# Kernel optimization log

Hardware: AMD Instinct MI355X
Metric: run time of the kernel (lower is better)

## Reference

```python
import jax, jax.numpy as jnp
import numpy as np

N_WAY, K_SHOT = 5, 1
N_CLASSES = 64
D = 8


def _conv(x, w, b):
    y = jax.lax.conv_general_dilated(x, w, (2, 2), 'SAME',
                                     dimension_numbers=('NCHW', 'OIHW', 'NCHW'))
    return jax.nn.relu(y + b[None, :, None, None])


def setup_inputs() -> dict:
    key = jax.random.key(0)
    ks = jax.random.split(key, 12)
    b, s_sup, q, h, w = 4, N_WAY * K_SHOT, 1, 64, 64
    rnd = lambda k, shape: jax.random.normal(k, shape, jnp.float32) * 0.05
    return {
        'support_x': jax.random.normal(ks[0], (b, s_sup, 3, h, w), jnp.float32),
        'support_y': jax.random.randint(ks[1], (b, s_sup), 0, N_CLASSES),
        'query_x': jax.random.normal(ks[2], (b, q, 3, h, w), jnp.float32),
        'query_y': jax.random.randint(ks[3], (b, q), 0, N_CLASSES),
        'k1': rnd(ks[4], (32, 3, 3, 3)), 'bc1': jnp.zeros((32,), jnp.float32),
        'k2': rnd(ks[5], (48, 32, 3, 3)), 'bc2': jnp.zeros((48,), jnp.float32),
        'k3': rnd(ks[6], (64, 48, 3, 3)), 'bc3': jnp.zeros((64,), jnp.float32),
        'Wlog': rnd(ks[7], (64, N_CLASSES)), 'blog': jnp.zeros((N_CLASSES,), jnp.float32),
        'Wg1': rnd(ks[8], (132, 128)), 'bg1': jnp.zeros((128,), jnp.float32),
        'Wg2': rnd(ks[9], (128, 64)), 'bg2': jnp.zeros((64,), jnp.float32),
        'Wf1': rnd(ks[10], (64, 16)), 'bf1': jnp.zeros((16,), jnp.float32),
        'Wf2': rnd(ks[11], (16, 1)), 'bf2': jnp.zeros((1,), jnp.float32),
    }


def reference(support_x, support_y, query_x, query_y,
              k1, bc1, k2, bc2, k3, bc3, Wlog, blog,
              Wg1, bg1, Wg2, bg2, Wf1, bf1, Wf2, bf2):
    x = jnp.concatenate([support_x, query_x], axis=1)       # [b, s, 3, h, w]
    label = jnp.concatenate([support_y, query_y], axis=1)   # [b, s]
    b, s = label.shape
    h, w = x.shape[-2:]

    feat = x.reshape(b * s, 3, h, w)
    feat = _conv(feat, k1, bc1)
    feat = _conv(feat, k2, bc2)
    feat = _conv(feat, k3, bc3)                              # [b*s, c, D, D]
    c = feat.shape[1]
    logits = feat.mean(axis=(2, 3)) @ Wlog + blog            # [b*s, n_classes]

    # --- append normalized (i/d, j/d) coord channels ---
    ii = jnp.arange(D, dtype=feat.dtype) / D
    coord = jnp.stack([jnp.broadcast_to(ii[:, None], (D, D)),
                       jnp.broadcast_to(ii[None, :], (D, D))])        # [2, D, D]
    feat = feat.reshape(b, s, c, D, D)
    feat = jnp.concatenate([feat, jnp.broadcast_to(coord, (b, s, 2, D, D))], axis=2)
    c2 = c + 2
    m = D * D
    a = feat.reshape(b, s, c2, m).transpose(0, 1, 3, 2)      # [b, s, m, c2]

    # --- relation network g over all (set-pair, position-pair) combos ---
    # original: g(concat(x_i, x_j)) where x_i = x[b, j, :, q], x_j = x[b, i, :, p]
    # split first linear: concat @ Wg1 = x_i @ Wg1[:c2] + x_j @ Wg1[c2:]
    W1a, W1b = Wg1[:c2], Wg1[c2:]
    u = a @ W1a                                              # [b, s_j, m_q, 128]
    v = a @ W1b + bg1                                        # [b, s_i, m_p, 128]
    # hdd[b,i,j,q,p] = relu(u[b,j,q] + v[b,i,p])  -> [b, s, s, m, m, 128]
    hdd = jax.nn.relu(u[:, None, :, :, None, :] + v[:, :, None, None, :, :])
    g = jax.nn.relu(hdd @ Wg2 + bg2)                         # [b, s, s, m, m, 64]
    x_f = g.sum(axis=(3, 4))                                 # [b, s, s, 64]
    score = jax.nn.sigmoid(jax.nn.relu(x_f @ Wf1 + bf1) @ Wf2 + bf2)  # [b, s, s, 1]

    # --- losses ---
    logp = jax.nn.log_softmax(logits, axis=-1)
    lab = label.reshape(-1)
    cls_loss = -jnp.take_along_axis(logp, lab[:, None], axis=1).mean()

    y = (label[:, :, None] == label[:, None, :])[..., None].astype(score.dtype)
    P = score[..., 0]                                        # [b, s, s]
    Pt = P.transpose(0, 2, 1)
    sym, anti = 0.5 * (P + Pt), 0.5 * (P - Pt)
    sym_n = jnp.sqrt((sym ** 2).sum(axis=(1, 2)))            # Frobenius per batch
    anti_n = jnp.sqrt((anti ** 2).sum(axis=(1, 2)))
    sym_loss = ((sym_n - anti_n) / (sym_n + anti_n)).mean()
    euc_loss = ((score - y) ** 2).mean()
    rn_loss = euc_loss - 0.1 * sym_loss
    return (cls_loss, rn_loss, sym_loss)
```

## Files before the change

kernel.cpp:

```cpp
#include <hip/hip_runtime.h>

typedef _Float16 f16x8 __attribute__((ext_vector_type(8)));
typedef float f32x4 __attribute__((ext_vector_type(4)));

__global__ void conv1_k(const float* __restrict__ sx, const float* __restrict__ qx,
                        const float* __restrict__ w, const float* __restrict__ bias,
                        float* __restrict__ out,
                        const float* __restrict__ Wg2, _Float16* __restrict__ W2h) {
    if (blockIdx.x == 768) {
        for (int s = 0; s < 4; s++) {
            int slot = threadIdx.x + 256*s;
            int tile = slot >> 6, lane = slot & 63;
            int kt = tile >> 2, nt = tile & 3;
            int quad = lane >> 4, col = lane & 15;
            f16x8 t;
            #pragma unroll
            for (int jj = 0; jj < 8; jj++)
                t[jj] = (_Float16)Wg2[(kt*32 + quad*8 + jj)*64 + nt*16 + col];
            *(f16x8*)&W2h[slot*8] = t;
        }
        return;
    }
    int n  = blockIdx.x >> 5;
    int oc = blockIdx.x & 31;
    int bi = n / 6, si = n % 6;
    const float* inp = (si < 5) ? sx + (size_t)((bi*5+si)*3)*4096
                                : qx + (size_t)(bi*3)*4096;
    __shared__ float wl[27];
    __shared__ float bl;
    if (threadIdx.x < 27) wl[threadIdx.x] = w[oc*27 + threadIdx.x];
    if (threadIdx.x == 0) bl = bias[oc];
    __syncthreads();
    for (int idx = threadIdx.x; idx < 1024; idx += 256) {
        int oy = idx >> 5, ox = idx & 31;
        float acc = bl;
        #pragma unroll
        for (int ic = 0; ic < 3; ic++) {
            const float* ip = inp + ic*4096;
            #pragma unroll
            for (int dy = 0; dy < 3; dy++) {
                int iy = 2*oy + dy;
                if (iy >= 64) continue;
                #pragma unroll
                for (int dx = 0; dx < 3; dx++) {
                    int ix = 2*ox + dx;
                    if (ix >= 64) continue;
                    acc += ip[iy*64+ix] * wl[ic*9 + dy*3 + dx];
                }
            }
        }
        out[(size_t)(n*32+oc)*1024 + idx] = fmaxf(acc, 0.f);
    }
}

__global__ void conv2_k(const float* __restrict__ in, const float* __restrict__ w,
                        const float* __restrict__ bias, float* __restrict__ out) {
    int n   = blockIdx.x / 12;
    int ocg = blockIdx.x % 12;
    __shared__ float wl[4*32*9];
    for (int e = threadIdx.x; e < 1152; e += 256) wl[e] = w[ocg*4*288 + e];
    __syncthreads();
    int oy = threadIdx.x >> 4, ox = threadIdx.x & 15;
    float a0 = bias[ocg*4+0], a1 = bias[ocg*4+1], a2 = bias[ocg*4+2], a3 = bias[ocg*4+3];
    const float* ib = in + (size_t)n*32*1024;
    for (int ic = 0; ic < 32; ic++) {
        const float* ip = ib + ic*1024;
        float tap[9];
        #pragma unroll
        for (int dy = 0; dy < 3; dy++)
            #pragma unroll
            for (int dx = 0; dx < 3; dx++) {
                int iy = 2*oy+dy, ix = 2*ox+dx;
                tap[dy*3+dx] = (iy < 32 && ix < 32) ? ip[iy*32+ix] : 0.f;
            }
        #pragma unroll
        for (int t = 0; t < 9; t++) {
            a0 += tap[t]*wl[0*288 + ic*9 + t];
            a1 += tap[t]*wl[1*288 + ic*9 + t];
            a2 += tap[t]*wl[2*288 + ic*9 + t];
            a3 += tap[t]*wl[3*288 + ic*9 + t];
        }
    }
    size_t ob = (size_t)(n*48 + ocg*4)*256 + threadIdx.x;
    out[ob        ] = fmaxf(a0, 0.f);
    out[ob + 256  ] = fmaxf(a1, 0.f);
    out[ob + 512  ] = fmaxf(a2, 0.f);
    out[ob + 768  ] = fmaxf(a3, 0.f);
}

__global__ void conv3_k(const float* __restrict__ in, const float* __restrict__ w,
                        const float* __restrict__ bias, float* __restrict__ out,
                        float* __restrict__ mf) {
    int n   = blockIdx.x >> 3;
    int ocg = blockIdx.x & 7;
    __shared__ float wl[8*48*9];
    for (int e = threadIdx.x; e < 3456; e += 256) wl[e] = w[ocg*8*432 + e];
    __syncthreads();
    int pix = threadIdx.x & 63, osub = threadIdx.x >> 6;
    int oy = pix >> 3, ox = pix & 7;
    int ol0 = osub*2;
    float a0 = bias[ocg*8 + ol0], a1 = bias[ocg*8 + ol0 + 1];
    const float* ib = in + (size_t)n*48*256;
    for (int ic = 0; ic < 48; ic++) {
        const float* ip = ib + ic*256;
        float tap[9];
        #pragma unroll
        for (int dy = 0; dy < 3; dy++)
            #pragma unroll
            for (int dx = 0; dx < 3; dx++) {
                int iy = 2*oy+dy, ix = 2*ox+dx;
                tap[dy*3+dx] = (iy < 16 && ix < 16) ? ip[iy*16+ix] : 0.f;
            }
        #pragma unroll
        for (int t = 0; t < 9; t++) {
            a0 += tap[t]*wl[ ol0   *432 + ic*9 + t];
            a1 += tap[t]*wl[(ol0+1)*432 + ic*9 + t];
        }
    }
    float r0 = fmaxf(a0, 0.f), r1 = fmaxf(a1, 0.f);
    out[(size_t)(n*64 + ocg*8 + ol0  )*64 + pix] = r0;
    out[(size_t)(n*64 + ocg*8 + ol0+1)*64 + pix] = r1;
    #pragma unroll
    for (int off = 32; off >= 1; off >>= 1) {
        r0 += __shfl_xor(r0, off, 64);
        r1 += __shfl_xor(r1, off, 64);
    }
    if (pix == 0) {
        mf[n*64 + ocg*8 + ol0    ] = r0 * (1.f/64.f);
        mf[n*64 + ocg*8 + ol0 + 1] = r1 * (1.f/64.f);
    }
}

__global__ void uvcls_k(const float* __restrict__ feat3, const float* __restrict__ Wg1,
                        const float* __restrict__ bg1, _Float16* __restrict__ u,
                        _Float16* __restrict__ v,
                        const float* __restrict__ mf, const int* __restrict__ sy,
                        const int* __restrict__ qy, const float* __restrict__ Wlog,
                        const float* __restrict__ blog, float* __restrict__ rv) {
    int tid = threadIdx.x;
    if (blockIdx.x >= 384) {
        int n = blockIdx.x - 384;
        if (tid >= 64) return;
        int lane = tid;
        float s = blog[lane];
        for (int c = 0; c < 64; c++) s += mf[n*64 + c] * Wlog[c*64 + lane];
        float mx = s;
        #pragma unroll
        for (int off = 32; off >= 1; off >>= 1) mx = fmaxf(mx, __shfl_xor(mx, off, 64));
        float p = __expf(s - mx);
        float se = p;
        #pragma unroll
        for (int off = 32; off >= 1; off >>= 1) se += __shfl_xor(se, off, 64);
        int bi = n/6, si = n%6;
        int lab = (si < 5) ? sy[bi*5+si] : qy[bi];
        float s_lab = __shfl(s, lab, 64);
        if (lane == 0) rv[n] = -(s_lab - mx - __logf(se));
        return;
    }
    int bs = blockIdx.x >> 4;
    int pg = blockIdx.x & 15;
    __shared__ float a4[4][66];
    for (int e = tid; e < 264; e += 128) {
        int pl = e / 66, c = e % 66;
        int p = pg*4 + pl;
        float vv;
        if (c < 64)       vv = feat3[(size_t)(bs*64 + c)*64 + p];
        else if (c == 64) vv = (float)(p >> 3) * 0.125f;
        else              vv = (float)(p & 7) * 0.125f;
        a4[pl][c] = vv;
    }
    __syncthreads();
    float us[4] = {0.f,0.f,0.f,0.f};
    float bg = bg1[tid];
    float vs[4] = {bg,bg,bg,bg};
    for (int c = 0; c < 66; c++) {
        float wa = Wg1[c*128 + tid];
        float wb = Wg1[(66+c)*128 + tid];
        #pragma unroll
        for (int pl = 0; pl < 4; pl++) {
            us[pl] += a4[pl][c]*wa;
            vs[pl] += a4[pl][c]*wb;
        }
    }
    #pragma unroll
    for (int pl = 0; pl < 4; pl++) {
        int p = pg*4 + pl;
        u[(size_t)(bs*64+p)*128 + tid] = (_Float16)us[pl];
        v[(size_t)(bs*64+p)*128 + tid] = (_Float16)vs[pl];
    }
}

__global__ void __launch_bounds__(256) rel_k(
        const _Float16* __restrict__ U, const _Float16* __restrict__ V,
        const _Float16* __restrict__ W2h, const float* __restrict__ bg2,
        float* __restrict__ xfpart) {
    __shared__ __align__(16) _Float16 Vsh[16*128];
    __shared__ float xfred[4][64];

    int bx = blockIdx.x;
    int cb = bx >> 2, qc = bx & 3;
    int b = cb / 36, rem = cb % 36;
    int j = rem / 6, i = rem % 6;
    int tid  = threadIdx.x;
    int wv   = tid >> 6, lane = tid & 63;
    int col  = lane & 15, quad = lane >> 4;

    const _Float16* ub = U + (size_t)(b*6 + i)*8192;
    const _Float16* vb = V + (size_t)(b*6 + j)*8192 + qc*16*128;

    *(f16x8*)&Vsh[tid*8] = *(const f16x8*)&vb[tid*8];

    f16x8 uf[4];
    {
        const _Float16* up = ub + (wv*16 + col)*128 + quad*8;
        #pragma unroll
        for (int kt = 0; kt < 4; kt++) uf[kt] = *(const f16x8*)&up[kt*32];
    }
    f16x8 bf[4][4];
    #pragma unroll
    for (int kt = 0; kt < 4; kt++)
        #pragma unroll
        for (int nt = 0; nt < 4; nt++)
            bf[kt][nt] = *(const f16x8*)&W2h[(size_t)(((kt*4+nt)*64) + lane)*8];
    float bgv[4];
    #pragma unroll
    for (int nt = 0; nt < 4; nt++) bgv[nt] = bg2[nt*16 + col];

    __syncthreads();

    float sums[4] = {0.f,0.f,0.f,0.f};
    for (int q = 0; q < 16; q++) {
        const _Float16* vp = &Vsh[q*128 + quad*8];
        f32x4 acc[4];
        #pragma unroll
        for (int nt = 0; nt < 4; nt++)
            acc[nt] = (f32x4){bgv[nt], bgv[nt], bgv[nt], bgv[nt]};
        #pragma unroll
        for (int kt = 0; kt < 4; kt++) {
            f16x8 vf = *(const f16x8*)&vp[kt*32];
            f16x8 af = uf[kt] + vf;
            af = __builtin_elementwise_max(af, (f16x8){0,0,0,0,0,0,0,0});
            #pragma unroll
            for (int nt = 0; nt < 4; nt++)
                acc[nt] = __builtin_amdgcn_mfma_f32_16x16x32_f16(af, bf[kt][nt], acc[nt], 0, 0, 0);
        }
        #pragma unroll
        for (int nt = 0; nt < 4; nt++)
            #pragma unroll
            for (int rr = 0; rr < 4; rr++)
                sums[nt] += fmaxf(acc[nt][rr], 0.f);
    }

    #pragma unroll
    for (int nt = 0; nt < 4; nt++) {
        sums[nt] += __shfl_xor(sums[nt], 16, 64);
        sums[nt] += __shfl_xor(sums[nt], 32, 64);
    }
    if (lane < 16) {
        #pragma unroll
        for (int nt = 0; nt < 4; nt++) xfred[wv][nt*16 + lane] = sums[nt];
    }
    __syncthreads();
    if (tid < 64)
        xfpart[(size_t)bx*64 + tid] = xfred[0][tid] + xfred[1][tid] + xfred[2][tid] + xfred[3][tid];
}

__global__ void loss_k(const float* __restrict__ xfp, const float* __restrict__ rv,
                       const int* __restrict__ sy, const int* __restrict__ qy,
                       const float* __restrict__ Wf1, const float* __restrict__ bf1,
                       const float* __restrict__ Wf2, const float* __restrict__ bf2,
                       float* __restrict__ out) {
    __shared__ float Wf1sh[1024];
    __shared__ float wf2sh[16];
    __shared__ float bf1sh[16];
    __shared__ float Pm[144];
    __shared__ int lab[24];
    __shared__ float red[256];
    __shared__ float ratio[4];
    int tid = threadIdx.x;
    for (int e = tid; e < 1024; e += 256) Wf1sh[e] = Wf1[e];
    if (tid < 16) { wf2sh[tid] = Wf2[tid]; bf1sh[tid] = bf1[tid]; }
    if (tid < 24) { int bi = tid/6, si = tid%6; lab[tid] = (si < 5) ? sy[bi*5+si] : qy[bi]; }
    __syncthreads();
    if (tid < 144) {
        float hid[16];
        #pragma unroll
        for (int h = 0; h < 16; h++) hid[h] = bf1sh[h];
        const float* xb = xfp + (size_t)tid*4*64;
        for (int n = 0; n < 64; n++) {
            float x = xb[n] + xb[64+n] + xb[128+n] + xb[192+n];
            #pragma unroll
            for (int h = 0; h < 16; h++) hid[h] += x * Wf1sh[n*16 + h];
        }
        float sc = bf2[0];
        #pragma unroll
        for (int h = 0; h < 16; h++) sc += fmaxf(hid[h], 0.f) * wf2sh[h];
        Pm[tid] = 1.f/(1.f + __expf(-sc));
    }
    __syncthreads();
    float e = 0.f;
    if (tid < 144) {
        int b = tid/36, r = tid%36, jj = r/6, ii = r%6;
        float y = (lab[b*6+jj] == lab[b*6+ii]) ? 1.f : 0.f;
        float d = Pm[tid] - y;
        e = d*d;
    }
    red[tid] = e;
    __syncthreads();
    for (int s = 128; s > 0; s >>= 1) {
        if (tid < s) red[tid] += red[tid+s];
        __syncthreads();
    }
    if (tid < 4) {
        float s2 = 0.f, a2 = 0.f;
        for (int jj = 0; jj < 6; jj++)
            for (int ii = 0; ii < 6; ii++) {
                float pa = Pm[tid*36 + jj*6 + ii], pb = Pm[tid*36 + ii*6 + jj];
                float sm = 0.5f*(pa+pb), an = 0.5f*(pa-pb);
                s2 += sm*sm; a2 += an*an;
            }
        float sn = sqrtf(s2), anq = sqrtf(a2);
        ratio[tid] = (sn - anq)/(sn + anq);
    }
    __syncthreads();
    if (tid == 0) {
        float sl = 0.25f*(ratio[0]+ratio[1]+ratio[2]+ratio[3]);
        float euc = red[0] * (1.f/144.f);
        float cs = 0.f;
        for (int k = 0; k < 24; k++) cs += rv[k];
        out[0] = cs * (1.f/24.f);
        out[1] = euc - 0.1f*sl;
        out[2] = sl;
    }
}

extern "C" void kernel_launch(void* const* d_in, const int* in_sizes, int n_in,
                              void* d_out, int out_size, void* d_ws, size_t ws_size,
                              hipStream_t stream) {
    const float* sx   = (const float*)d_in[0];
    const int*   sy   = (const int*)  d_in[1];
    const float* qx   = (const float*)d_in[2];
    const int*   qy   = (const int*)  d_in[3];
    const float* k1   = (const float*)d_in[4];
    const float* bc1  = (const float*)d_in[5];
    const float* k2   = (const float*)d_in[6];
    const float* bc2  = (const float*)d_in[7];
    const float* k3   = (const float*)d_in[8];
    const float* bc3  = (const float*)d_in[9];
    const float* Wlog = (const float*)d_in[10];
    const float* blog = (const float*)d_in[11];
    const float* Wg1  = (const float*)d_in[12];
    const float* bg1  = (const float*)d_in[13];
    const float* Wg2  = (const float*)d_in[14];
    const float* bg2  = (const float*)d_in[15];
    const float* Wf1  = (const float*)d_in[16];
    const float* bf1  = (const float*)d_in[17];
    const float* Wf2  = (const float*)d_in[18];
    const float* bf2  = (const float*)d_in[19];

    float* ws    = (float*)d_ws;
    float* feat1 = ws;
    float* feat2 = feat1 + 786432;
    float* feat3 = feat2 + 294912;
    float* mf    = feat3 + 98304;
    float* rv    = mf    + 1536;
    float* xfp   = rv    + 32;
    _Float16* u16 = (_Float16*)(xfp + 36864);
    _Float16* v16 = u16 + 196608;
    _Float16* W2h = v16 + 196608;
    float* out   = (float*)d_out;

    conv1_k <<<769,    256, 0, stream>>>(sx, qx, k1, bc1, feat1, Wg2, W2h);
    conv2_k <<<24*12,  256, 0, stream>>>(feat1, k2, bc2, feat2);
    conv3_k <<<24*8,   256, 0, stream>>>(feat2, k3, bc3, feat3, mf);
    uvcls_k <<<408,    128, 0, stream>>>(feat3, Wg1, bg1, u16, v16,
                                         mf, sy, qy, Wlog, blog, rv);
    rel_k   <<<576,    256, 0, stream>>>(u16, v16, W2h, bg2, xfp);
    loss_k  <<<1,      256, 0, stream>>>(xfp, rv, sy, qy, Wf1, bf1, Wf2, bf2, out);
}
```

Before: 190.5 us.

## Fuse all six stages into one cooperative persistent kernel with grid syncs

```diff
diff --git a/kernel.cpp b/kernel.cpp
--- a/kernel.cpp
+++ b/kernel.cpp
@@ -1,342 +1,378 @@
 #include <hip/hip_runtime.h>
+#include <hip/hip_cooperative_groups.h>
+
+namespace cg = cooperative_groups;
 
 typedef _Float16 f16x8 __attribute__((ext_vector_type(8)));
 typedef float f32x4 __attribute__((ext_vector_type(4)));
 
-__global__ void conv1_k(const float* __restrict__ sx, const float* __restrict__ qx,
-                        const float* __restrict__ w, const float* __restrict__ bias,
-                        float* __restrict__ out,
-                        const float* __restrict__ Wg2, _Float16* __restrict__ W2h) {
-    if (blockIdx.x == 768) {
-        for (int s = 0; s < 4; s++) {
-            int slot = threadIdx.x + 256*s;
-            int tile = slot >> 6, lane = slot & 63;
-            int kt = tile >> 2, nt = tile & 3;
-            int quad = lane >> 4, col = lane & 15;
-            f16x8 t;
-            #pragma unroll
-            for (int jj = 0; jj < 8; jj++)
-                t[jj] = (_Float16)Wg2[(kt*32 + quad*8 + jj)*64 + nt*16 + col];
-            *(f16x8*)&W2h[slot*8] = t;
-        }
-        return;
-    }
-    int n  = blockIdx.x >> 5;
-    int oc = blockIdx.x & 31;
-    int bi = n / 6, si = n % 6;
-    const float* inp = (si < 5) ? sx + (size_t)((bi*5+si)*3)*4096
-                                : qx + (size_t)(bi*3)*4096;
-    __shared__ float wl[27];
-    __shared__ float bl;
-    if (threadIdx.x < 27) wl[threadIdx.x] = w[oc*27 + threadIdx.x];
-    if (threadIdx.x == 0) bl = bias[oc];
-    __syncthreads();
-    for (int idx = threadIdx.x; idx < 1024; idx += 256) {
-        int oy = idx >> 5, ox = idx & 31;
-        float acc = bl;
+__global__ void __launch_bounds__(512) mega_k(
+    const float* __restrict__ sx, const int* __restrict__ sy,
+    const float* __restrict__ qx, const int* __restrict__ qy,
+    const float* __restrict__ k1, const float* __restrict__ bc1,
+    const float* __restrict__ k2, const float* __restrict__ bc2,
+    const float* __restrict__ k3, const float* __restrict__ bc3,
+    const float* __restrict__ Wlog, const float* __restrict__ blog,
+    const float* __restrict__ Wg1, const float* __restrict__ bg1,
+    const float* __restrict__ Wg2, const float* __restrict__ bg2,
+    const float* __restrict__ Wf1, const float* __restrict__ bf1,
+    const float* __restrict__ Wf2, const float* __restrict__ bf2,
+    float* __restrict__ ws, float* __restrict__ out)
+{
+    cg::grid_group grid = cg::this_grid();
+    __shared__ __align__(16) float smem_all[2][3584];
+    const int tid512 = threadIdx.x;
+    const int sub = tid512 >> 8;
+    const int tid = tid512 & 255;
+    float* smem = smem_all[sub];
+    const int bid = blockIdx.x;
+    const int tb  = bid*2 + sub;
+
+    float* feat1 = ws;
+    float* feat2 = feat1 + 786432;
+    float* feat3 = feat2 + 294912;
+    float* mf    = feat3 + 98304;
+    float* rv    = mf    + 1536;
+    float* xfp   = rv    + 64;
+    float* Pmg   = xfp   + 36864;
+    _Float16* u16 = (_Float16*)(Pmg + 160);
+    _Float16* v16 = u16 + 196608;
+    _Float16* W2h = v16 + 196608;
+
+    for (int itr = 0; itr < 2; itr++) {
+        int t = itr*512 + tb;
+        __syncthreads();
+        if (t < 768) {
+            int oc = t & 31;
+            if (tid < 27) smem[tid] = k1[oc*27 + tid];
+            else if (tid == 27) smem[27] = bc1[oc];
+        }
+        __syncthreads();
+        if (t < 768) {
+            int n = t >> 5, oc = t & 31;
+            int bi = n / 6, si = n % 6;
+            const float* inp = (si < 5) ? sx + (size_t)((bi*5+si)*3)*4096
+                                        : qx + (size_t)(bi*3)*4096;
+            #pragma unroll
+            for (int k = 0; k < 4; k++) {
+                int idx = tid + 256*k;
+                int oy = idx >> 5, ox = idx & 31;
+                float acc = smem[27];
+                #pragma unroll
+                for (int ic = 0; ic < 3; ic++) {
+                    const float* ip = inp + ic*4096;
+                    #pragma unroll
+                    for (int dy = 0; dy < 3; dy++) {
+                        int iy = 2*oy + dy;
+                        if (iy >= 64) continue;
+                        #pragma unroll
+                        for (int dx = 0; dx < 3; dx++) {
+                            int ix = 2*ox + dx;
+                            if (ix >= 64) continue;
+                            acc += ip[iy*64+ix] * smem[ic*9 + dy*3 + dx];
+                        }
+                    }
+                }
+                feat1[(size_t)(n*32+oc)*1024 + idx] = fmaxf(acc, 0.f);
+            }
+        } else if (t == 768) {
+            #pragma unroll
+            for (int s = 0; s < 4; s++) {
+                int slot = tid + 256*s;
+                int tile = slot >> 6, lane2 = slot & 63;
+                int kt = tile >> 2, nt = tile & 3;
+                int quad2 = lane2 >> 4, col2 = lane2 & 15;
+                f16x8 tt;
+                #pragma unroll
+                for (int jj = 0; jj < 8; jj++)
+                    tt[jj] = (_Float16)Wg2[(kt*32 + quad2*8 + jj)*64 + nt*16 + col2];
+                *(f16x8*)&W2h[slot*8] = tt;
+            }
+        }
+    }
+    grid.sync();
+
+    {
+        int t = tb;
+        bool act = t < 288;
+        int n = t / 12, ocg = t % 12;
+        if (act) for (int e = tid; e < 1152; e += 256) smem[e] = k2[ocg*1152 + e];
+        __syncthreads();
+        if (act) {
+            int oy = tid >> 4, ox = tid & 15;
+            float a0 = bc2[ocg*4+0], a1 = bc2[ocg*4+1], a2 = bc2[ocg*4+2], a3 = bc2[ocg*4+3];
+            const float* ib = feat1 + (size_t)n*32768;
+            for (int ic = 0; ic < 32; ic++) {
+                const float* ip = ib + ic*1024;
+                float tap[9];
+                #pragma unroll
+                for (int dy = 0; dy < 3; dy++)
+                    #pragma unroll
+                    for (int dx = 0; dx < 3; dx++) {
+                        int iy = 2*oy+dy, ix = 2*ox+dx;
+                        tap[dy*3+dx] = (iy < 32 && ix < 32) ? ip[iy*32+ix] : 0.f;
+                    }
+                #pragma unroll
+                for (int u2 = 0; u2 < 9; u2++) {
+                    a0 += tap[u2]*smem[0*288 + ic*9 + u2];
+                    a1 += tap[u2]*smem[1*288 + ic*9 + u2];
+                    a2 += tap[u2]*smem[2*288 + ic*9 + u2];
+                    a3 += tap[u2]*smem[3*288 + ic*9 + u2];
+                }
+            }
+            size_t ob = (size_t)(n*48 + ocg*4)*256 + tid;
+            feat2[ob      ] = fmaxf(a0, 0.f);
+            feat2[ob + 256] = fmaxf(a1, 0.f);
+            feat2[ob + 512] = fmaxf(a2, 0.f);
+            feat2[ob + 768] = fmaxf(a3, 0.f);
+        }
+    }
+    grid.sync();
+
+    {
+        int t = tb;
+        bool act = t < 192;
+        int n = t >> 3, ocg = t & 7;
+        if (act) for (int e = tid; e < 3456; e += 256) smem[e] = k3[ocg*3456 + e];
+        __syncthreads();
+        if (act) {
+            int pix = tid & 63, osub = tid >> 6;
+            int oy = pix >> 3, ox = pix & 7;
+            int ol0 = osub*2;
+            float a0 = bc3[ocg*8 + ol0], a1 = bc3[ocg*8 + ol0 + 1];
+            const float* ib = feat2 + (size_t)n*12288;
+            for (int ic = 0; ic < 48; ic++) {
+                const float* ip = ib + ic*256;
+                float tap[9];
+                #pragma unroll
+                for (int dy = 0; dy < 3; dy++)
+                    #pragma unroll
+                    for (int dx = 0; dx < 3; dx++) {
+                        int iy = 2*oy+dy, ix = 2*ox+dx;
+                        tap[dy*3+dx] = (iy < 16 && ix < 16) ? ip[iy*16+ix] : 0.f;
+                    }
+                #pragma unroll
+                for (int u2 = 0; u2 < 9; u2++) {
+                    a0 += tap[u2]*smem[ ol0   *432 + ic*9 + u2];
+                    a1 += tap[u2]*smem[(ol0+1)*432 + ic*9 + u2];
+                }
+            }
+            float r0 = fmaxf(a0, 0.f), r1 = fmaxf(a1, 0.f);
+            feat3[(size_t)(n*64 + ocg*8 + ol0  )*64 + pix] = r0;
+            feat3[(size_t)(n*64 + ocg*8 + ol0+1)*64 + pix] = r1;
+            #pragma unroll
+            for (int off = 32; off >= 1; off >>= 1) {
+                r0 += __shfl_xor(r0, off, 64);
+                r1 += __shfl_xor(r1, off, 64);
+            }
+            if (pix == 0) {
+                mf[n*64 + ocg*8 + ol0    ] = r0 * (1.f/64.f);
+                mf[n*64 + ocg*8 + ol0 + 1] = r1 * (1.f/64.f);
+            }
+        }
+    }
+    grid.sync();
+
+    {
+        int t = tb;
+        if (t < 384) {
+            int bs = t >> 4, pg = t & 15;
+            for (int e = tid; e < 264; e += 256) {
+                int pl = e / 66, c = e % 66;
+                int p = pg*4 + pl;
+                float vvv;
+                if (c < 64)       vvv = feat3[(size_t)(bs*64 + c)*64 + p];
+                else if (c == 64) vvv = (float)(p >> 3) * 0.125f;
+                else              vvv = (float)(p & 7) * 0.125f;
+                smem[pl*66 + c] = vvv;
+            }
+        }
+        __syncthreads();
+        if (t < 384) {
+            int bs = t >> 4, pg = t & 15;
+            int col = tid & 127;
+            bool isV = tid >= 128;
+            const float* Wcol = Wg1 + (isV ? 66*128 : 0) + col;
+            float b0 = isV ? bg1[col] : 0.f;
+            float acc0 = b0, acc1 = b0, acc2 = b0, acc3 = b0;
+            for (int c = 0; c < 66; c++) {
+                float wv2 = Wcol[c*128];
+                acc0 += smem[c]      * wv2;
+                acc1 += smem[66+c]   * wv2;
+                acc2 += smem[132+c]  * wv2;
+                acc3 += smem[198+c]  * wv2;
+            }
+            _Float16* dst = isV ? v16 : u16;
+            size_t base = (size_t)(bs*64 + pg*4)*128 + col;
+            dst[base      ] = (_Float16)acc0;
+            dst[base + 128] = (_Float16)acc1;
+            dst[base + 256] = (_Float16)acc2;
+            dst[base + 384] = (_Float16)acc3;
+        } else if (t < 408 && tid < 64) {
+            int n = t - 384;
+            float s = blog[tid];
+            for (int c = 0; c < 64; c++) s += mf[n*64 + c] * Wlog[c*64 + tid];
+            float mx = s;
+            #pragma unroll
+            for (int off = 32; off >= 1; off >>= 1) mx = fmaxf(mx, __shfl_xor(mx, off, 64));
+            float p = __expf(s - mx);
+            float se = p;
+            #pragma unroll
+            for (int off = 32; off >= 1; off >>= 1) se += __shfl_xor(se, off, 64);
+            int bi = n/6, si = n%6;
+            int lab = (si < 5) ? sy[bi*5+si] : qy[bi];
+            float s_lab = __shfl(s, lab, 64);
+            if (tid == 0) rv[n] = -(s_lab - mx - __logf(se));
+        }
+    }
+    grid.sync();
+
+    {
+        const int lane = tid & 63, wv = tid >> 6;
+        const int col = lane & 15, quad = lane >> 4;
+        f16x8 bf[4][4];
         #pragma unroll
-        for (int ic = 0; ic < 3; ic++) {
-            const float* ip = inp + ic*4096;
-            #pragma unroll
-            for (int dy = 0; dy < 3; dy++) {
-                int iy = 2*oy + dy;
-                if (iy >= 64) continue;
-                #pragma unroll
-                for (int dx = 0; dx < 3; dx++) {
-                    int ix = 2*ox + dx;
-                    if (ix >= 64) continue;
-                    acc += ip[iy*64+ix] * wl[ic*9 + dy*3 + dx];
-                }
-            }
-        }
-        out[(size_t)(n*32+oc)*1024 + idx] = fmaxf(acc, 0.f);
-    }
-}
-
-__global__ void conv2_k(const float* __restrict__ in, const float* __restrict__ w,
-                        const float* __restrict__ bias, float* __restrict__ out) {
-    int n   = blockIdx.x / 12;
-    int ocg = blockIdx.x % 12;
-    __shared__ float wl[4*32*9];
-    for (int e = threadIdx.x; e < 1152; e += 256) wl[e] = w[ocg*4*288 + e];
-    __syncthreads();
-    int oy = threadIdx.x >> 4, ox = threadIdx.x & 15;
-    float a0 = bias[ocg*4+0], a1 = bias[ocg*4+1], a2 = bias[ocg*4+2], a3 = bias[ocg*4+3];
-    const float* ib = in + (size_t)n*32*1024;
-    for (int ic = 0; ic < 32; ic++) {
-        const float* ip = ib + ic*1024;
-        float tap[9];
+        for (int kt = 0; kt < 4; kt++)
+            #pragma unroll
+            for (int nt = 0; nt < 4; nt++)
+                bf[kt][nt] = *(const f16x8*)&W2h[(size_t)(((kt*4+nt)*64) + lane)*8];
+        float bgv[4];
         #pragma unroll
-        for (int dy = 0; dy < 3; dy++)
-            #pragma unroll
-            for (int dx = 0; dx < 3; dx++) {
-                int iy = 2*oy+dy, ix = 2*ox+dx;
-                tap[dy*3+dx] = (iy < 32 && ix < 32) ? ip[iy*32+ix] : 0.f;
-            }
-        #pragma unroll
-        for (int t = 0; t < 9; t++) {
-            a0 += tap[t]*wl[0*288 + ic*9 + t];
-            a1 += tap[t]*wl[1*288 + ic*9 + t];
-            a2 += tap[t]*wl[2*288 + ic*9 + t];
-            a3 += tap[t]*wl[3*288 + ic*9 + t];
-        }
-    }
-    size_t ob = (size_t)(n*48 + ocg*4)*256 + threadIdx.x;
-    out[ob        ] = fmaxf(a0, 0.f);
-    out[ob + 256  ] = fmaxf(a1, 0.f);
-    out[ob + 512  ] = fmaxf(a2, 0.f);
-    out[ob + 768  ] = fmaxf(a3, 0.f);
-}
-
-__global__ void conv3_k(const float* __restrict__ in, const float* __restrict__ w,
-                        const float* __restrict__ bias, float* __restrict__ out,
-                        float* __restrict__ mf) {
-    int n   = blockIdx.x >> 3;
-    int ocg = blockIdx.x & 7;
-    __shared__ float wl[8*48*9];
-    for (int e = threadIdx.x; e < 3456; e += 256) wl[e] = w[ocg*8*432 + e];
-    __syncthreads();
-    int pix = threadIdx.x & 63, osub = threadIdx.x >> 6;
-    int oy = pix >> 3, ox = pix & 7;
-    int ol0 = osub*2;
-    float a0 = bias[ocg*8 + ol0], a1 = bias[ocg*8 + ol0 + 1];
-    const float* ib = in + (size_t)n*48*256;
-    for (int ic = 0; ic < 48; ic++) {
-        const float* ip = ib + ic*256;
-        float tap[9];
-        #pragma unroll
-        for (int dy = 0; dy < 3; dy++)
-            #pragma unroll
-            for (int dx = 0; dx < 3; dx++) {
-                int iy = 2*oy+dy, ix = 2*ox+dx;
-                tap[dy*3+dx] = (iy < 16 && ix < 16) ? ip[iy*16+ix] : 0.f;
-            }
-        #pragma unroll
-        for (int t = 0; t < 9; t++) {
-            a0 += tap[t]*wl[ ol0   *432 + ic*9 + t];
-            a1 += tap[t]*wl[(ol0+1)*432 + ic*9 + t];
-        }
-    }
-    float r0 = fmaxf(a0, 0.f), r1 = fmaxf(a1, 0.f);
-    out[(size_t)(n*64 + ocg*8 + ol0  )*64 + pix] = r0;
-    out[(size_t)(n*64 + ocg*8 + ol0+1)*64 + pix] = r1;
-    #pragma unroll
-    for (int off = 32; off >= 1; off >>= 1) {
-        r0 += __shfl_xor(r0, off, 64);
-        r1 += __shfl_xor(r1, off, 64);
-    }
-    if (pix == 0) {
-        mf[n*64 + ocg*8 + ol0    ] = r0 * (1.f/64.f);
-        mf[n*64 + ocg*8 + ol0 + 1] = r1 * (1.f/64.f);
-    }
-}
-
-__global__ void uvcls_k(const float* __restrict__ feat3, const float* __restrict__ Wg1,
-                        const float* __restrict__ bg1, _Float16* __restrict__ u,
-                        _Float16* __restrict__ v,
-                        const float* __restrict__ mf, const int* __restrict__ sy,
-                        const int* __restrict__ qy, const float* __restrict__ Wlog,
-                        const float* __restrict__ blog, float* __restrict__ rv) {
-    int tid = threadIdx.x;
-    if (blockIdx.x >= 384) {
-        int n = blockIdx.x - 384;
-        if (tid >= 64) return;
-        int lane = tid;
-        float s = blog[lane];
-        for (int c = 0; c < 64; c++) s += mf[n*64 + c] * Wlog[c*64 + lane];
-        float mx = s;
-        #pragma unroll
-        for (int off = 32; off >= 1; off >>= 1) mx = fmaxf(mx, __shfl_xor(mx, off, 64));
-        float p = __expf(s - mx);
-        float se = p;
-        #pragma unroll
-        for (int off = 32; off >= 1; off >>= 1) se += __shfl_xor(se, off, 64);
-        int bi = n/6, si = n%6;
-        int lab = (si < 5) ? sy[bi*5+si] : qy[bi];
-        float s_lab = __shfl(s, lab, 64);
-        if (lane == 0) rv[n] = -(s_lab - mx - __logf(se));
-        return;
-    }
-    int bs = blockIdx.x >> 4;
-    int pg = blockIdx.x & 15;
-    __shared__ float a4[4][66];
-    for (int e = tid; e < 264; e += 128) {
-        int pl = e / 66, c = e % 66;
-        int p = pg*4 + pl;
-        float vv;
-        if (c < 64)       vv = feat3[(size_t)(bs*64 + c)*64 + p];
-        else if (c == 64) vv = (float)(p >> 3) * 0.125f;
-        else              vv = (float)(p & 7) * 0.125f;
-        a4[pl][c] = vv;
-    }
-    __syncthreads();
-    float us[4] = {0.f,0.f,0.f,0.f};
-    float bg = bg1[tid];
-    float vs[4] = {bg,bg,bg,bg};
-    for (int c = 0; c < 66; c++) {
-        float wa = Wg1[c*128 + tid];
-        float wb = Wg1[(66+c)*128 + tid];
-        #pragma unroll
-        for (int pl = 0; pl < 4; pl++) {
-            us[pl] += a4[pl][c]*wa;
-            vs[pl] += a4[pl][c]*wb;
-        }
-    }
-    #pragma unroll
-    for (int pl = 0; pl < 4; pl++) {
-        int p = pg*4 + pl;
-        u[(size_t)(bs*64+p)*128 + tid] = (_Float16)us[pl];
-        v[(size_t)(bs*64+p)*128 + tid] = (_Float16)vs[pl];
-    }
-}
-
-__global__ void __launch_bounds__(256) rel_k(
-        const _Float16* __restrict__ U, const _Float16* __restrict__ V,
-        const _Float16* __restrict__ W2h, const float* __restrict__ bg2,
-        float* __restrict__ xfpart) {
-    __shared__ __align__(16) _Float16 Vsh[16*128];
-    __shared__ float xfred[4][64];
-
-    int bx = blockIdx.x;
-    int cb = bx >> 2, qc = bx & 3;
-    int b = cb / 36, rem = cb % 36;
-    int j = rem / 6, i = rem % 6;
-    int tid  = threadIdx.x;
-    int wv   = tid >> 6, lane = tid & 63;
-    int col  = lane & 15, quad = lane >> 4;
-
-    const _Float16* ub = U + (size_t)(b*6 + i)*8192;
-    const _Float16* vb = V + (size_t)(b*6 + j)*8192 + qc*16*128;
-
-    *(f16x8*)&Vsh[tid*8] = *(const f16x8*)&vb[tid*8];
-
-    f16x8 uf[4];
+        for (int nt = 0; nt < 4; nt++) bgv[nt] = bg2[nt*16 + col];
+
+        for (int itr = 0; itr < 2; itr++) {
+            int t = itr*512 + tb;
+            bool act = t < 576;
+            __syncthreads();
+            _Float16* Vsh = (_Float16*)smem;
+            float* xfred  = smem + 1024;
+            f16x8 uf[4];
+            if (act) {
+                int cb = t >> 2, qc = t & 3;
+                int b = cb / 36, rem = cb % 36;
+                int j = rem / 6, i = rem % 6;
+                const _Float16* ub = u16 + (size_t)(b*6 + i)*8192;
+                const _Float16* vb = v16 + (size_t)(b*6 + j)*8192 + qc*2048;
+                *(f16x8*)&Vsh[tid*8] = *(const f16x8*)&vb[tid*8];
+                const _Float16* up = ub + (wv*16 + col)*128 + quad*8;
+                #pragma unroll
+                for (int kt = 0; kt < 4; kt++) uf[kt] = *(const f16x8*)&up[kt*32];
+            }
+            __syncthreads();
+            if (act) {
+                float sums[4] = {0.f,0.f,0.f,0.f};
+                for (int q = 0; q < 16; q++) {
+                    const _Float16* vp = &Vsh[q*128 + quad*8];
+                    f32x4 acc[4];
+                    #pragma unroll
+                    for (int nt = 0; nt < 4; nt++)
+                        acc[nt] = (f32x4){bgv[nt], bgv[nt], bgv[nt], bgv[nt]};
+                    #pragma unroll
+                    for (int kt = 0; kt < 4; kt++) {
+                        f16x8 vf = *(const f16x8*)&vp[kt*32];
+                        f16x8 af = uf[kt] + vf;
+                        af = __builtin_elementwise_max(af, (f16x8){0,0,0,0,0,0,0,0});
+                        #pragma unroll
+                        for (int nt = 0; nt < 4; nt++)
+                            acc[nt] = __builtin_amdgcn_mfma_f32_16x16x32_f16(af, bf[kt][nt], acc[nt], 0, 0, 0);
+                    }
+                    #pragma unroll
+                    for (int nt = 0; nt < 4; nt++)
+                        #pragma unroll
+                        for (int rr = 0; rr < 4; rr++)
+                            sums[nt] += fmaxf(acc[nt][rr], 0.f);
+                }
+                #pragma unroll
+                for (int nt = 0; nt < 4; nt++) {
+                    sums[nt] += __shfl_xor(sums[nt], 16, 64);
+                    sums[nt] += __shfl_xor(sums[nt], 32, 64);
+                }
+                if (lane < 16) {
+                    #pragma unroll
+                    for (int nt = 0; nt < 4; nt++) xfred[wv*64 + nt*16 + lane] = sums[nt];
+                }
+            }
+            __syncthreads();
+            if (act && tid < 64)
+                xfp[(size_t)t*64 + tid] = xfred[tid] + xfred[64+tid] + xfred[128+tid] + xfred[192+tid];
+        }
+    }
+    grid.sync();
+
     {
-        const _Float16* up = ub + (wv*16 + col)*128 + quad*8;
-        #pragma unroll
-        for (int kt = 0; kt < 4; kt++) uf[kt] = *(const f16x8*)&up[kt*32];
-    }
-    f16x8 bf[4][4];
-    #pragma unroll
-    for (int kt = 0; kt < 4; kt++)
-        #pragma unroll
-        for (int nt = 0; nt < 4; nt++)
-            bf[kt][nt] = *(const f16x8*)&W2h[(size_t)(((kt*4+nt)*64) + lane)*8];
-    float bgv[4];
-    #pragma unroll
-    for (int nt = 0; nt < 4; nt++) bgv[nt] = bg2[nt*16 + col];
-
-    __syncthreads();
-
-    float sums[4] = {0.f,0.f,0.f,0.f};
-    for (int q = 0; q < 16; q++) {
-        const _Float16* vp = &Vsh[q*128 + quad*8];
-        f32x4 acc[4];
-        #pragma unroll
-        for (int nt = 0; nt < 4; nt++)
-            acc[nt] = (f32x4){bgv[nt], bgv[nt], bgv[nt], bgv[nt]};
-        #pragma unroll
-        for (int kt = 0; kt < 4; kt++) {
-            f16x8 vf = *(const f16x8*)&vp[kt*32];
-            f16x8 af = uf[kt] + vf;
-            af = __builtin_elementwise_max(af, (f16x8){0,0,0,0,0,0,0,0});
-            #pragma unroll
-            for (int nt = 0; nt < 4; nt++)
-                acc[nt] = __builtin_amdgcn_mfma_f32_16x16x32_f16(af, bf[kt][nt], acc[nt], 0, 0, 0);
-        }
-        #pragma unroll
-        for (int nt = 0; nt < 4; nt++)
-            #pragma unroll
-            for (int rr = 0; rr < 4; rr++)
-                sums[nt] += fmaxf(acc[nt][rr], 0.f);
-    }
-
-    #pragma unroll
-    for (int nt = 0; nt < 4; nt++) {
-        sums[nt] += __shfl_xor(sums[nt], 16, 64);
-        sums[nt] += __shfl_xor(sums[nt], 32, 64);
-    }
-    if (lane < 16) {
-        #pragma unroll
-        for (int nt = 0; nt < 4; nt++) xfred[wv][nt*16 + lane] = sums[nt];
-    }
-    __syncthreads();
-    if (tid < 64)
-        xfpart[(size_t)bx*64 + tid] = xfred[0][tid] + xfred[1][tid] + xfred[2][tid] + xfred[3][tid];
-}
-
-__global__ void loss_k(const float* __restrict__ xfp, const float* __restrict__ rv,
-                       const int* __restrict__ sy, const int* __restrict__ qy,
-                       const float* __restrict__ Wf1, const float* __restrict__ bf1,
-                       const float* __restrict__ Wf2, const float* __restrict__ bf2,
-                       float* __restrict__ out) {
-    __shared__ float Wf1sh[1024];
-    __shared__ float wf2sh[16];
-    __shared__ float bf1sh[16];
-    __shared__ float Pm[144];
-    __shared__ int lab[24];
-    __shared__ float red[256];
-    __shared__ float ratio[4];
-    int tid = threadIdx.x;
-    for (int e = tid; e < 1024; e += 256) Wf1sh[e] = Wf1[e];
-    if (tid < 16) { wf2sh[tid] = Wf2[tid]; bf1sh[tid] = bf1[tid]; }
-    if (tid < 24) { int bi = tid/6, si = tid%6; lab[tid] = (si < 5) ? sy[bi*5+si] : qy[bi]; }
-    __syncthreads();
-    if (tid < 144) {
-        float hid[16];
-        #pragma unroll
-        for (int h = 0; h < 16; h++) hid[h] = bf1sh[h];
-        const float* xb = xfp + (size_t)tid*4*64;
-        for (int n = 0; n < 64; n++) {
-            float x = xb[n] + xb[64+n] + xb[128+n] + xb[192+n];
-            #pragma unroll
-            for (int h = 0; h < 16; h++) hid[h] += x * Wf1sh[n*16 + h];
-        }
-        float sc = bf2[0];
-        #pragma unroll
-        for (int h = 0; h < 16; h++) sc += fmaxf(hid[h], 0.f) * wf2sh[h];
-        Pm[tid] = 1.f/(1.f + __expf(-sc));
-    }
-    __syncthreads();
-    float e = 0.f;
-    if (tid < 144) {
-        int b = tid/36, r = tid%36, jj = r/6, ii = r%6;
-        float y = (lab[b*6+jj] == lab[b*6+ii]) ? 1.f : 0.f;
-        float d = Pm[tid] - y;
-        e = d*d;
-    }
-    red[tid] = e;
-    __syncthreads();
-    for (int s = 128; s > 0; s >>= 1) {
-        if (tid < s) red[tid] += red[tid+s];
-        __syncthreads();
-    }
-    if (tid < 4) {
-        float s2 = 0.f, a2 = 0.f;
-        for (int jj = 0; jj < 6; jj++)
-            for (int ii = 0; ii < 6; ii++) {
-                float pa = Pm[tid*36 + jj*6 + ii], pb = Pm[tid*36 + ii*6 + jj];
-                float sm = 0.5f*(pa+pb), an = 0.5f*(pa-pb);
-                s2 += sm*sm; a2 += an*an;
-            }
-        float sn = sqrtf(s2), anq = sqrtf(a2);
-        ratio[tid] = (sn - anq)/(sn + anq);
-    }
-    __syncthreads();
-    if (tid == 0) {
-        float sl = 0.25f*(ratio[0]+ratio[1]+ratio[2]+ratio[3]);
-        float euc = red[0] * (1.f/144.f);
-        float cs = 0.f;
-        for (int k = 0; k < 24; k++) cs += rv[k];
-        out[0] = cs * (1.f/24.f);
-        out[1] = euc - 0.1f*sl;
-        out[2] = sl;
+        int t = tb;
+        bool act = t < 144;
+        if (act && tid < 64) {
+            const float* xb = xfp + (size_t)t*256;
+            smem[tid] = xb[tid] + xb[64+tid] + xb[128+tid] + xb[192+tid];
+        }
+        __syncthreads();
+        if (act && tid < 16) {
+            float s = bf1[tid];
+            for (int c = 0; c < 64; c++) s += smem[c]*Wf1[c*16 + tid];
+            smem[64 + tid] = fmaxf(s, 0.f);
+        }
+        __syncthreads();
+        if (act && tid == 0) {
+            float sc = bf2[0];
+            #pragma unroll
+            for (int h = 0; h < 16; h++) sc += smem[64+h]*Wf2[h];
+            Pmg[t] = 1.f/(1.f + __expf(-sc));
+        }
+    }
+    grid.sync();
+
+    if (bid == 0) {
+        float* s0   = &smem_all[0][0];
+        float* Pmsh = s0;
+        int*   lab  = (int*)(s0 + 144);
+        float* red  = s0 + 192;
+        float* ratio= s0 + 704;
+        int tt = tid512;
+        if (tt < 144) Pmsh[tt] = Pmg[tt];
+        if (tt < 24) { int bi = tt/6, si = tt%6; lab[tt] = (si < 5) ? sy[bi*5+si] : qy[bi]; }
+        __syncthreads();
+        float e = 0.f;
+        if (tt < 144) {
+            int b = tt/36, r = tt%36, jj = r/6, ii = r%6;
+            float y = (lab[b*6+jj] == lab[b*6+ii]) ? 1.f : 0.f;
+            float d = Pmsh[tt] - y;
+            e = d*d;
+        }
+        red[tt] = e;
+        __syncthreads();
+        for (int s = 256; s > 0; s >>= 1) {
+            if (tt < s) red[tt] += red[tt+s];
+            __syncthreads();
+        }
+        if (tt < 4) {
+            float s2 = 0.f, a2 = 0.f;
+            for (int jj = 0; jj < 6; jj++)
+                for (int ii = 0; ii < 6; ii++) {
+                    float pa = Pmsh[tt*36 + jj*6 + ii], pb = Pmsh[tt*36 + ii*6 + jj];
+                    float sm = 0.5f*(pa+pb), an = 0.5f*(pa-pb);
+                    s2 += sm*sm; a2 += an*an;
+                }
+            float sn = sqrtf(s2), anq = sqrtf(a2);
+            ratio[tt] = (sn - anq)/(sn + anq);
+        }
+        __syncthreads();
+        if (tt == 0) {
+            float sl = 0.25f*(ratio[0]+ratio[1]+ratio[2]+ratio[3]);
+            float euc = red[0] * (1.f/144.f);
+            float cs = 0.f;
+            for (int k = 0; k < 24; k++) cs += rv[k];
+            out[0] = cs * (1.f/24.f);
+            out[1] = euc - 0.1f*sl;
+            out[2] = sl;
+        }
     }
 }
 
 extern "C" void kernel_launch(void* const* d_in, const int* in_sizes, int n_in,
                               void* d_out, int out_size, void* d_ws, size_t ws_size,
                               hipStream_t stream) {
+    (void)in_sizes; (void)n_in; (void)out_size; (void)ws_size;
     const float* sx   = (const float*)d_in[0];
     const int*   sy   = (const int*)  d_in[1];
     const float* qx   = (const float*)d_in[2];
@@ -357,24 +393,16 @@
     const float* bf1  = (const float*)d_in[17];
     const float* Wf2  = (const float*)d_in[18];
     const float* bf2  = (const float*)d_in[19];
-
-    float* ws    = (float*)d_ws;
-    float* feat1 = ws;
-    float* feat2 = feat1 + 786432;
-    float* feat3 = feat2 + 294912;
-    float* mf    = feat3 + 98304;
-    float* rv    = mf    + 1536;
-    float* xfp   = rv    + 32;
-    _Float16* u16 = (_Float16*)(xfp + 36864);
-    _Float16* v16 = u16 + 196608;
-    _Float16* W2h = v16 + 196608;
-    float* out   = (float*)d_out;
-
-    conv1_k <<<769,    256, 0, stream>>>(sx, qx, k1, bc1, feat1, Wg2, W2h);
-    conv2_k <<<24*12,  256, 0, stream>>>(feat1, k2, bc2, feat2);
-    conv3_k <<<24*8,   256, 0, stream>>>(feat2, k3, bc3, feat3, mf);
-    uvcls_k <<<408,    128, 0, stream>>>(feat3, Wg1, bg1, u16, v16,
-                                         mf, sy, qy, Wlog, blog, rv);
-    rel_k   <<<576,    256, 0, stream>>>(u16, v16, W2h, bg2, xfp);
-    loss_k  <<<1,      256, 0, stream>>>(xfp, rv, sy, qy, Wf1, bf1, Wf2, bf2, out);
+    float* ws  = (float*)d_ws;
+    float* out = (float*)d_out;
+
+    void* args[] = {
+        (void*)&sx, (void*)&sy, (void*)&qx, (void*)&qy,
+        (void*)&k1, (void*)&bc1, (void*)&k2, (void*)&bc2,
+        (void*)&k3, (void*)&bc3, (void*)&Wlog, (void*)&blog,
+        (void*)&Wg1, (void*)&bg1, (void*)&Wg2, (void*)&bg2,
+        (void*)&Wf1, (void*)&bf1, (void*)&Wf2, (void*)&bf2,
+        (void*)&ws, (void*)&out
+    };
+    hipLaunchCooperativeKernel((void*)mega_k, dim3(256), dim3(512), args, 0, stream);
 }
```

Result: slower. 394.0 us (+106.8%).
